# Performance work log

Measured on AMD Instinct MI355X. Metric: run time of the kernel, lower is better.

Reference implementation:

```python
import math
import jax, jax.numpy as jnp
import numpy as np

N_HEAD = 1
NORM_GROUPS = 32
EPS = 1e-5


def setup_inputs() -> dict:
    key = jax.random.key(0)
    ks = jax.random.split(key, 3)
    B, C, H, W, L = 4, 64, 16, 16, 16
    x = jax.random.normal(ks[0], (B, C, H, W, L), dtype=jnp.float32)
    gn_weight = jnp.ones((C,), dtype=jnp.float32)
    gn_bias = jnp.zeros((C,), dtype=jnp.float32)
    # 1x1x1 conv == per-voxel matmul; init like torch conv (kaiming-ish scale)
    qkv_weight = jax.random.normal(ks[1], (3 * C, C), dtype=jnp.float32) / math.sqrt(C)
    out_weight = jax.random.normal(ks[2], (C, C), dtype=jnp.float32) / math.sqrt(C)
    out_bias = jnp.zeros((C,), dtype=jnp.float32)
    return {"x": x, "gn_weight": gn_weight, "gn_bias": gn_bias,
            "qkv_weight": qkv_weight, "out_weight": out_weight, "out_bias": out_bias}


def _group_norm(x, w, b):
    B, C, H, W, L = x.shape
    g = NORM_GROUPS
    xg = x.reshape(B, g, C // g, H, W, L)
    mean = xg.mean(axis=(2, 3, 4, 5), keepdims=True)
    var = xg.var(axis=(2, 3, 4, 5), keepdims=True)
    xn = ((xg - mean) * jax.lax.rsqrt(var + EPS)).reshape(B, C, H, W, L)
    return xn * w[None, :, None, None, None] + b[None, :, None, None, None]


def reference(x, gn_weight, gn_bias, qkv_weight, out_weight, out_bias):
    B, C, H, W, L = x.shape
    n_head = N_HEAD
    head_dim = C // n_head
    N = H * W * L  # flattened voxel count

    norm = _group_norm(x, gn_weight, gn_bias)
    # 1x1x1 conv C -> 3C (no bias), then split heads
    qkv = jnp.einsum('bchwl,dc->bdhwl', norm, qkv_weight)
    qkv = qkv.reshape(B, n_head, 3 * head_dim, N)
    q, k, v = jnp.split(qkv, 3, axis=2)  # each [B, n_head, head_dim, N]

    # full N^2 attention; scale by sqrt(channel) as in the original (NOT head_dim)
    attn = jnp.einsum('bncq,bnck->bnqk', q, k) / math.sqrt(C)
    attn = jax.nn.softmax(attn, axis=-1)
    out = jnp.einsum('bnqk,bnck->bncq', attn, v).reshape(B, C, H, W, L)

    out = jnp.einsum('bchwl,dc->bdhwl', out, out_weight) + out_bias[None, :, None, None, None]
    return out + x
```

## Files before the change

### kernel.cpp

```cpp
#include <hip/hip_runtime.h>
#include <hip/hip_bf16.h>
#include <math.h>

#define BATCH 4
#define CH    64
#define NVOX  4096
#define NGRP  32
#define EPS   1e-5f

typedef float f32x4 __attribute__((ext_vector_type(4)));
typedef short s16x8 __attribute__((ext_vector_type(8)));

static __device__ inline unsigned short f2bf(float f) {
    union { __hip_bfloat16 h; unsigned short u; } cv;
    cv.h = __float2bfloat16(f);
    return cv.u;
}

__global__ __launch_bounds__(256) void k_gnstats(const float* __restrict__ x,
                                                 float* __restrict__ stats) {
    int bg = blockIdx.x;
    const float4* p4 = (const float4*)(x + (size_t)bg * (2 * NVOX));
    float s = 0.f, sq = 0.f;
    for (int i = threadIdx.x; i < (2 * NVOX) / 4; i += 256) {
        float4 v = p4[i];
        s  += v.x + v.y + v.z + v.w;
        sq += v.x * v.x + v.y * v.y + v.z * v.z + v.w * v.w;
    }
    for (int off = 32; off; off >>= 1) {
        s  += __shfl_down(s, off);
        sq += __shfl_down(sq, off);
    }
    __shared__ float ls[4], lq[4];
    int wid = threadIdx.x >> 6;
    if ((threadIdx.x & 63) == 0) { ls[wid] = s; lq[wid] = sq; }
    __syncthreads();
    if (threadIdx.x == 0) {
        s  = ls[0] + ls[1] + ls[2] + ls[3];
        sq = lq[0] + lq[1] + lq[2] + lq[3];
        float mean = s / (float)(2 * NVOX);
        float var  = sq / (float)(2 * NVOX) - mean * mean;
        stats[bg]       = mean;
        stats[128 + bg] = rsqrtf(var + EPS);
    }
}

__global__ __launch_bounds__(256) void k_qkv(const float* __restrict__ x,
                                             const float* __restrict__ stats,
                                             const float* __restrict__ gw,
                                             const float* __restrict__ gb,
                                             const float* __restrict__ W,
                                             unsigned short* __restrict__ Qb,
                                             unsigned short* __restrict__ Kb,
                                             unsigned short* __restrict__ Vb) {
    int b  = blockIdx.x >> 6;
    int n0 = (blockIdx.x & 63) * 64;
    int t  = threadIdx.x;
    __shared__ float nm[64][64];
    __shared__ alignas(16) unsigned short tb[64][72];

    for (int i = t; i < 64 * 16; i += 256) {
        int c = i >> 4;
        int n = (i & 15) * 4;
        float4 v = *(const float4*)&x[((size_t)(b * CH + c)) * NVOX + n0 + n];
        float mean = stats[b * NGRP + (c >> 1)];
        float rstd = stats[128 + b * NGRP + (c >> 1)];
        float sc = rstd * gw[c];
        float sh = gb[c] - mean * sc;
        nm[c][n + 0] = v.x * sc + sh;
        nm[c][n + 1] = v.y * sc + sh;
        nm[c][n + 2] = v.z * sc + sh;
        nm[c][n + 3] = v.w * sc + sh;
    }
    __syncthreads();

    int nl = t & 63;
    int dg = t >> 6;
    float r[64];
    #pragma unroll
    for (int c = 0; c < 64; ++c) r[c] = nm[c][nl];

    for (int j = 0; j < 16; ++j) {
        int d = dg * 16 + j;
        const float* w = &W[d * 64];
        float acc = 0.f;
        #pragma unroll
        for (int c = 0; c < 64; ++c) acc += w[c] * r[c];
        tb[nl][d] = f2bf(acc * 0.125f);
    }
    __syncthreads();
    {
        int n = t >> 2, d0 = (t & 3) * 16;
        s16x8 a0 = *(const s16x8*)&tb[n][d0];
        s16x8 a1 = *(const s16x8*)&tb[n][d0 + 8];
        size_t base = ((size_t)(b * NVOX + n0 + n)) * 64 + d0;
        *(s16x8*)&Qb[base]     = a0;
        *(s16x8*)&Qb[base + 8] = a1;
    }
    __syncthreads();

    for (int j = 0; j < 16; ++j) {
        int d = dg * 16 + j;
        const float* w = &W[(64 + d) * 64];
        float acc = 0.f;
        #pragma unroll
        for (int c = 0; c < 64; ++c) acc += w[c] * r[c];
        tb[nl][d] = f2bf(acc);
    }
    __syncthreads();
    {
        int n = t >> 2, d0 = (t & 3) * 16;
        s16x8 a0 = *(const s16x8*)&tb[n][d0];
        s16x8 a1 = *(const s16x8*)&tb[n][d0 + 8];
        size_t base = ((size_t)(b * NVOX + n0 + n)) * 64 + d0;
        *(s16x8*)&Kb[base]     = a0;
        *(s16x8*)&Kb[base + 8] = a1;
    }

    for (int j = 0; j < 16; ++j) {
        int d = dg * 16 + j;
        const float* w = &W[(128 + d) * 64];
        float acc = 0.f;
        #pragma unroll
        for (int c = 0; c < 64; ++c) acc += w[c] * r[c];
        Vb[((size_t)(b * 64 + d)) * NVOX + n0 + nl] = f2bf(acc);
    }
}

__global__ __launch_bounds__(256) void k_attn(const unsigned short* __restrict__ Qb,
                                              const unsigned short* __restrict__ Kb,
                                              const unsigned short* __restrict__ Vb,
                                              float* __restrict__ Obuf) {
    int b    = blockIdx.x >> 6;
    int q0   = (blockIdx.x & 63) * 64;
    int t    = threadIdx.x;
    int lane = t & 63;
    int w    = t >> 6;

    __shared__ alignas(16) unsigned short Ks[64][72];
    __shared__ alignas(16) unsigned short Vs[64][72];
    __shared__ alignas(16) unsigned short Ps[4][16][72];

    const unsigned short* Qp = Qb + (size_t)b * NVOX * 64;
    const unsigned short* Kp = Kb + (size_t)b * NVOX * 64;
    const unsigned short* Vp = Vb + (size_t)b * 64 * NVOX;

    int l15 = lane & 15;
    int g4  = lane >> 4;
    int csl = g4 * 8;
    int qrow = q0 + w * 16 + l15;
    s16x8 qf0 = *(const s16x8*)&Qp[(size_t)qrow * 64 + csl];
    s16x8 qf1 = *(const s16x8*)&Qp[(size_t)qrow * 64 + csl + 32];

    f32x4 acc_o[4] = {};
    float m_r[4], l_r[4];
    #pragma unroll
    for (int i = 0; i < 4; ++i) { m_r[i] = -1e30f; l_r[i] = 0.f; }

    int sr = t >> 2;
    int sc = (t & 3) * 16;

    s16x8 kr0, kr1, vr0, vr1;
    {
        const s16x8* pk = (const s16x8*)&Kp[(size_t)sr * 64 + sc];
        kr0 = pk[0]; kr1 = pk[1];
        const s16x8* pv = (const s16x8*)&Vp[(size_t)sr * NVOX + sc];
        vr0 = pv[0]; vr1 = pv[1];
    }

    for (int it = 0; it < NVOX / 64; ++it) {
        *(s16x8*)&Ks[sr][sc]     = kr0;
        *(s16x8*)&Ks[sr][sc + 8] = kr1;
        *(s16x8*)&Vs[sr][sc]     = vr0;
        *(s16x8*)&Vs[sr][sc + 8] = vr1;
        __syncthreads();

        if (it < NVOX / 64 - 1) {
            int k0n = (it + 1) * 64;
            const s16x8* pk = (const s16x8*)&Kp[((size_t)(k0n + sr)) * 64 + sc];
            kr0 = pk[0]; kr1 = pk[1];
            const s16x8* pv = (const s16x8*)&Vp[(size_t)sr * NVOX + k0n + sc];
            vr0 = pv[0]; vr1 = pv[1];
        }

        f32x4 sacc[4];
        #pragma unroll
        for (int kt = 0; kt < 4; ++kt) {
            s16x8 kf0 = *(const s16x8*)&Ks[kt * 16 + l15][csl];
            s16x8 kf1 = *(const s16x8*)&Ks[kt * 16 + l15][csl + 32];
            f32x4 z = {0.f, 0.f, 0.f, 0.f};
            sacc[kt] = __builtin_amdgcn_mfma_f32_16x16x32_bf16(qf0, kf0, z, 0, 0, 0);
            sacc[kt] = __builtin_amdgcn_mfma_f32_16x16x32_bf16(qf1, kf1, sacc[kt], 0, 0, 0);
        }

        float al[4];
        #pragma unroll
        for (int reg = 0; reg < 4; ++reg) {
            float rmax = fmaxf(fmaxf(sacc[0][reg], sacc[1][reg]),
                               fmaxf(sacc[2][reg], sacc[3][reg]));
            rmax = fmaxf(rmax, __shfl_xor(rmax, 1));
            rmax = fmaxf(rmax, __shfl_xor(rmax, 2));
            rmax = fmaxf(rmax, __shfl_xor(rmax, 4));
            rmax = fmaxf(rmax, __shfl_xor(rmax, 8));
            float mn = fmaxf(m_r[reg], rmax);
            al[reg] = __expf(m_r[reg] - mn);
            m_r[reg] = mn;
        }
        float p[4][4];
        #pragma unroll
        for (int kt = 0; kt < 4; ++kt)
            #pragma unroll
            for (int reg = 0; reg < 4; ++reg)
                p[kt][reg] = __expf(sacc[kt][reg] - m_r[reg]);
        #pragma unroll
        for (int reg = 0; reg < 4; ++reg) {
            float rs = p[0][reg] + p[1][reg] + p[2][reg] + p[3][reg];
            rs += __shfl_xor(rs, 1);
            rs += __shfl_xor(rs, 2);
            rs += __shfl_xor(rs, 4);
            rs += __shfl_xor(rs, 8);
            l_r[reg] = l_r[reg] * al[reg] + rs;
        }
        #pragma unroll
        for (int kt = 0; kt < 4; ++kt)
            #pragma unroll
            for (int reg = 0; reg < 4; ++reg)
                Ps[w][g4 * 4 + reg][kt * 16 + l15] = f2bf(p[kt][reg]);
        #pragma unroll
        for (int ct = 0; ct < 4; ++ct)
            #pragma unroll
            for (int reg = 0; reg < 4; ++reg)
                acc_o[ct][reg] *= al[reg];

        s16x8 pf0 = *(const s16x8*)&Ps[w][l15][csl];
        s16x8 pf1 = *(const s16x8*)&Ps[w][l15][csl + 32];
        #pragma unroll
        for (int ct = 0; ct < 4; ++ct) {
            s16x8 vf0 = *(const s16x8*)&Vs[ct * 16 + l15][csl];
            s16x8 vf1 = *(const s16x8*)&Vs[ct * 16 + l15][csl + 32];
            acc_o[ct] = __builtin_amdgcn_mfma_f32_16x16x32_bf16(pf0, vf0, acc_o[ct], 0, 0, 0);
            acc_o[ct] = __builtin_amdgcn_mfma_f32_16x16x32_bf16(pf1, vf1, acc_o[ct], 0, 0, 0);
        }
        __syncthreads();
    }

    float inv[4];
    #pragma unroll
    for (int reg = 0; reg < 4; ++reg) inv[reg] = 1.f / l_r[reg];
    #pragma unroll
    for (int ct = 0; ct < 4; ++ct)
        #pragma unroll
        for (int reg = 0; reg < 4; ++reg) {
            int q = q0 + w * 16 + g4 * 4 + reg;
            Obuf[((size_t)(b * NVOX + q)) * 64 + ct * 16 + l15] =
                acc_o[ct][reg] * inv[reg];
        }
}

__global__ __launch_bounds__(256) void k_outproj(const float* __restrict__ Obuf,
                                                 const float* __restrict__ Wout,
                                                 const float* __restrict__ obias,
                                                 const float* __restrict__ x,
                                                 float* __restrict__ out) {
    int b  = blockIdx.x >> 6;
    int n0 = (blockIdx.x & 63) * 64;
    int t  = threadIdx.x;
    __shared__ float os[64][65];
    for (int i = t; i < 64 * 16; i += 256) {
        int n  = i >> 4;
        int c4 = (i & 15) * 4;
        float4 v = *(const float4*)&Obuf[((size_t)(b * NVOX + n0 + n)) * 64 + c4];
        os[n][c4 + 0] = v.x; os[n][c4 + 1] = v.y;
        os[n][c4 + 2] = v.z; os[n][c4 + 3] = v.w;
    }
    __syncthreads();
    int nl = t & 63;
    int dg = t >> 6;
    float r[64];
    #pragma unroll
    for (int c = 0; c < 64; ++c) r[c] = os[nl][c];
    for (int j = 0; j < 16; ++j) {
        int d = dg * 16 + j;
        const float* wv = &Wout[d * 64];
        float acc = obias[d];
        #pragma unroll
        for (int c = 0; c < 64; ++c) acc += wv[c] * r[c];
        size_t idx = ((size_t)(b * CH + d)) * NVOX + n0 + nl;
        out[idx] = acc + x[idx];
    }
}

extern "C" void kernel_launch(void* const* d_in, const int* in_sizes, int n_in,
                              void* d_out, int out_size, void* d_ws, size_t ws_size,
                              hipStream_t stream) {
    const float* x     = (const float*)d_in[0];
    const float* gw    = (const float*)d_in[1];
    const float* gb    = (const float*)d_in[2];
    const float* Wqkv  = (const float*)d_in[3];
    const float* Wout  = (const float*)d_in[4];
    const float* obias = (const float*)d_in[5];
    float* out = (float*)d_out;

    float* ws    = (float*)d_ws;
    float* stats = ws;
    unsigned short* Qb = (unsigned short*)(ws + 256);
    unsigned short* Kb = Qb + (size_t)BATCH * NVOX * 64;
    unsigned short* Vb = Kb + (size_t)BATCH * NVOX * 64;
    float* Obuf = (float*)(Vb + (size_t)BATCH * NVOX * 64);

    k_gnstats<<<BATCH * NGRP, 256, 0, stream>>>(x, stats);
    k_qkv   <<<BATCH * 64,   256, 0, stream>>>(x, stats, gw, gb, Wqkv, Qb, Kb, Vb);
    k_attn  <<<BATCH * 64,   256, 0, stream>>>(Qb, Kb, Vb, Obuf);
    k_outproj<<<BATCH * 64,  256, 0, stream>>>(Obuf, Wout, obias, x, out);
}
```

Before: 196.2 us.

## Split attention KV range four ways and merge partials in output projection

Attention work is split across four KV chunks, so the grid grows from 256 to 1024 blocks and fills more of the GPU's compute units. Each block writes its unnormalized output plus running max and sum. The output-projection kernel then rescales and combines the four partials before the matmul. This adds workspace traffic for four fp32 partial outputs. The change also adds partial-unroll pragmas on the projection loops.

```diff
diff --git a/kernel.cpp b/kernel.cpp
--- a/kernel.cpp
+++ b/kernel.cpp
@@ -7,6 +7,8 @@
 #define NVOX  4096
 #define NGRP  32
 #define EPS   1e-5f
+#define SPLITS 4
+#define KVS   (NVOX / SPLITS)
 
 typedef float f32x4 __attribute__((ext_vector_type(4)));
 typedef short s16x8 __attribute__((ext_vector_type(8)));
@@ -80,6 +82,7 @@
     #pragma unroll
     for (int c = 0; c < 64; ++c) r[c] = nm[c][nl];
 
+    #pragma unroll 4
     for (int j = 0; j < 16; ++j) {
         int d = dg * 16 + j;
         const float* w = &W[d * 64];
@@ -99,6 +102,7 @@
     }
     __syncthreads();
 
+    #pragma unroll 4
     for (int j = 0; j < 16; ++j) {
         int d = dg * 16 + j;
         const float* w = &W[(64 + d) * 64];
@@ -117,6 +121,7 @@
         *(s16x8*)&Kb[base + 8] = a1;
     }
 
+    #pragma unroll 4
     for (int j = 0; j < 16; ++j) {
         int d = dg * 16 + j;
         const float* w = &W[(128 + d) * 64];
@@ -130,12 +135,17 @@
 __global__ __launch_bounds__(256) void k_attn(const unsigned short* __restrict__ Qb,
                                               const unsigned short* __restrict__ Kb,
                                               const unsigned short* __restrict__ Vb,
-                                              float* __restrict__ Obuf) {
-    int b    = blockIdx.x >> 6;
-    int q0   = (blockIdx.x & 63) * 64;
-    int t    = threadIdx.x;
-    int lane = t & 63;
-    int w    = t >> 6;
+                                              float* __restrict__ Opart,
+                                              float* __restrict__ Mpart,
+                                              float* __restrict__ Lpart) {
+    int split = blockIdx.x & 3;
+    int bq    = blockIdx.x >> 2;
+    int b     = bq >> 6;
+    int q0    = (bq & 63) * 64;
+    int t     = threadIdx.x;
+    int lane  = t & 63;
+    int w     = t >> 6;
+    const int kbase = split * KVS;
 
     __shared__ alignas(16) unsigned short Ks[64][72];
     __shared__ alignas(16) unsigned short Vs[64][72];
@@ -162,21 +172,21 @@
 
     s16x8 kr0, kr1, vr0, vr1;
     {
-        const s16x8* pk = (const s16x8*)&Kp[(size_t)sr * 64 + sc];
+        const s16x8* pk = (const s16x8*)&Kp[((size_t)(kbase + sr)) * 64 + sc];
         kr0 = pk[0]; kr1 = pk[1];
-        const s16x8* pv = (const s16x8*)&Vp[(size_t)sr * NVOX + sc];
+        const s16x8* pv = (const s16x8*)&Vp[(size_t)sr * NVOX + kbase + sc];
         vr0 = pv[0]; vr1 = pv[1];
     }
 
-    for (int it = 0; it < NVOX / 64; ++it) {
+    for (int it = 0; it < KVS / 64; ++it) {
         *(s16x8*)&Ks[sr][sc]     = kr0;
         *(s16x8*)&Ks[sr][sc + 8] = kr1;
         *(s16x8*)&Vs[sr][sc]     = vr0;
         *(s16x8*)&Vs[sr][sc + 8] = vr1;
         __syncthreads();
 
-        if (it < NVOX / 64 - 1) {
-            int k0n = (it + 1) * 64;
+        if (it < KVS / 64 - 1) {
+            int k0n = kbase + (it + 1) * 64;
             const s16x8* pk = (const s16x8*)&Kp[((size_t)(k0n + sr)) * 64 + sc];
             kr0 = pk[0]; kr1 = pk[1];
             const s16x8* pv = (const s16x8*)&Vp[(size_t)sr * NVOX + k0n + sc];
@@ -244,20 +254,27 @@
         __syncthreads();
     }
 
-    float inv[4];
-    #pragma unroll
-    for (int reg = 0; reg < 4; ++reg) inv[reg] = 1.f / l_r[reg];
     #pragma unroll
     for (int ct = 0; ct < 4; ++ct)
         #pragma unroll
         for (int reg = 0; reg < 4; ++reg) {
             int q = q0 + w * 16 + g4 * 4 + reg;
-            Obuf[((size_t)(b * NVOX + q)) * 64 + ct * 16 + l15] =
-                acc_o[ct][reg] * inv[reg];
-        }
-}
-
-__global__ __launch_bounds__(256) void k_outproj(const float* __restrict__ Obuf,
+            Opart[(((size_t)split * BATCH + b) * NVOX + q) * 64 + ct * 16 + l15] =
+                acc_o[ct][reg];
+        }
+    if (l15 == 0) {
+        #pragma unroll
+        for (int reg = 0; reg < 4; ++reg) {
+            int q = q0 + w * 16 + g4 * 4 + reg;
+            Mpart[((size_t)split * BATCH + b) * NVOX + q] = m_r[reg];
+            Lpart[((size_t)split * BATCH + b) * NVOX + q] = l_r[reg];
+        }
+    }
+}
+
+__global__ __launch_bounds__(256) void k_outproj(const float* __restrict__ Opart,
+                                                 const float* __restrict__ Mpart,
+                                                 const float* __restrict__ Lpart,
                                                  const float* __restrict__ Wout,
                                                  const float* __restrict__ obias,
                                                  const float* __restrict__ x,
@@ -266,19 +283,48 @@
     int n0 = (blockIdx.x & 63) * 64;
     int t  = threadIdx.x;
     __shared__ float os[64][65];
+    __shared__ float scs[64][4];
+
+    if (t < 64) {
+        size_t qg = (size_t)b * NVOX + n0 + t;
+        float m[SPLITS], l[SPLITS];
+        #pragma unroll
+        for (int s = 0; s < SPLITS; ++s) {
+            m[s] = Mpart[(size_t)s * BATCH * NVOX + qg];
+            l[s] = Lpart[(size_t)s * BATCH * NVOX + qg];
+        }
+        float mm = fmaxf(fmaxf(m[0], m[1]), fmaxf(m[2], m[3]));
+        float e[SPLITS], lsum = 0.f;
+        #pragma unroll
+        for (int s = 0; s < SPLITS; ++s) { e[s] = __expf(m[s] - mm); lsum += l[s] * e[s]; }
+        float inv = 1.f / lsum;
+        #pragma unroll
+        for (int s = 0; s < SPLITS; ++s) scs[t][s] = e[s] * inv;
+    }
+    __syncthreads();
+
     for (int i = t; i < 64 * 16; i += 256) {
         int n  = i >> 4;
         int c4 = (i & 15) * 4;
-        float4 v = *(const float4*)&Obuf[((size_t)(b * NVOX + n0 + n)) * 64 + c4];
-        os[n][c4 + 0] = v.x; os[n][c4 + 1] = v.y;
-        os[n][c4 + 2] = v.z; os[n][c4 + 3] = v.w;
-    }
-    __syncthreads();
+        size_t base = ((size_t)(b * NVOX + n0 + n)) * 64 + c4;
+        float4 a = {0.f, 0.f, 0.f, 0.f};
+        #pragma unroll
+        for (int s = 0; s < SPLITS; ++s) {
+            float4 v = *(const float4*)&Opart[(size_t)s * BATCH * NVOX * 64 + base];
+            float f = scs[n][s];
+            a.x += f * v.x; a.y += f * v.y; a.z += f * v.z; a.w += f * v.w;
+        }
+        os[n][c4 + 0] = a.x; os[n][c4 + 1] = a.y;
+        os[n][c4 + 2] = a.z; os[n][c4 + 3] = a.w;
+    }
+    __syncthreads();
+
     int nl = t & 63;
     int dg = t >> 6;
     float r[64];
     #pragma unroll
     for (int c = 0; c < 64; ++c) r[c] = os[nl][c];
+    #pragma unroll 4
     for (int j = 0; j < 16; ++j) {
         int d = dg * 16 + j;
         const float* wv = &Wout[d * 64];
@@ -306,10 +352,12 @@
     unsigned short* Qb = (unsigned short*)(ws + 256);
     unsigned short* Kb = Qb + (size_t)BATCH * NVOX * 64;
     unsigned short* Vb = Kb + (size_t)BATCH * NVOX * 64;
-    float* Obuf = (float*)(Vb + (size_t)BATCH * NVOX * 64);
-
-    k_gnstats<<<BATCH * NGRP, 256, 0, stream>>>(x, stats);
-    k_qkv   <<<BATCH * 64,   256, 0, stream>>>(x, stats, gw, gb, Wqkv, Qb, Kb, Vb);
-    k_attn  <<<BATCH * 64,   256, 0, stream>>>(Qb, Kb, Vb, Obuf);
-    k_outproj<<<BATCH * 64,  256, 0, stream>>>(Obuf, Wout, obias, x, out);
-}
+    float* Opart = (float*)(Vb + (size_t)BATCH * NVOX * 64);
+    float* Mpart = Opart + (size_t)SPLITS * BATCH * NVOX * 64;
+    float* Lpart = Mpart + (size_t)SPLITS * BATCH * NVOX;
+
+    k_gnstats<<<BATCH * NGRP,        256, 0, stream>>>(x, stats);
+    k_qkv   <<<BATCH * 64,           256, 0, stream>>>(x, stats, gw, gb, Wqkv, Qb, Kb, Vb);
+    k_attn  <<<BATCH * 64 * SPLITS,  256, 0, stream>>>(Qb, Kb, Vb, Opart, Mpart, Lpart);
+    k_outproj<<<BATCH * 64,          256, 0, stream>>>(Opart, Mpart, Lpart, Wout, obias, x, out);
+}
```

Result: faster. 190.7 us (-2.8%).

## Split KV across waves, fuse output projection into attention, read K/V directly

Applied to the files above, without the earlier changes.

The attention kernel now gives each block 16 queries, with the four waves each handling a quarter of the key range (split-K flash attention). K and V fragments are loaded straight from global memory, so the shared-memory staging and per-iteration barriers are gone. The partial results are then merged through shared memory with a log-sum-exp combine, and the output 1x1 projection, bias and residual are applied in the same kernel, which removes the Obuf round trip and one launch. The grid grows to 1024 blocks with an XCD-style block swizzle, and the QKV loops get partial unrolling. The risks are redundant global/L2 reads of K and V, since each block rereads the whole K/V of its batch, and extra per-block merge work.

```diff
diff --git a/kernel.cpp b/kernel.cpp
--- a/kernel.cpp
+++ b/kernel.cpp
@@ -80,6 +80,7 @@
     #pragma unroll
     for (int c = 0; c < 64; ++c) r[c] = nm[c][nl];
 
+    #pragma unroll 4
     for (int j = 0; j < 16; ++j) {
         int d = dg * 16 + j;
         const float* w = &W[d * 64];
@@ -99,6 +100,7 @@
     }
     __syncthreads();
 
+    #pragma unroll 4
     for (int j = 0; j < 16; ++j) {
         int d = dg * 16 + j;
         const float* w = &W[(64 + d) * 64];
@@ -117,6 +119,7 @@
         *(s16x8*)&Kb[base + 8] = a1;
     }
 
+    #pragma unroll 4
     for (int j = 0; j < 16; ++j) {
         int d = dg * 16 + j;
         const float* w = &W[(128 + d) * 64];
@@ -127,67 +130,52 @@
     }
 }
 
-__global__ __launch_bounds__(256) void k_attn(const unsigned short* __restrict__ Qb,
-                                              const unsigned short* __restrict__ Kb,
-                                              const unsigned short* __restrict__ Vb,
-                                              float* __restrict__ Obuf) {
-    int b    = blockIdx.x >> 6;
-    int q0   = (blockIdx.x & 63) * 64;
+__global__ __launch_bounds__(256) void k_attn_fused(const unsigned short* __restrict__ Qb,
+                                                    const unsigned short* __restrict__ Kb,
+                                                    const unsigned short* __restrict__ Vb,
+                                                    const float* __restrict__ Wout,
+                                                    const float* __restrict__ obias,
+                                                    const float* __restrict__ x,
+                                                    float* __restrict__ out) {
+    int bid = blockIdx.x;
+    int swz = (bid & 7) * 128 + (bid >> 3);
+    int b   = swz >> 8;
+    int q0  = (swz & 255) * 16;
+
     int t    = threadIdx.x;
     int lane = t & 63;
     int w    = t >> 6;
-
-    __shared__ alignas(16) unsigned short Ks[64][72];
-    __shared__ alignas(16) unsigned short Vs[64][72];
+    int l15  = lane & 15;
+    int g4   = lane >> 4;
+    int csl  = g4 * 8;
+
     __shared__ alignas(16) unsigned short Ps[4][16][72];
+    __shared__ float Part[4][16][68];
+    __shared__ float ml[4][2][16];
+    __shared__ float Os[16][68];
 
     const unsigned short* Qp = Qb + (size_t)b * NVOX * 64;
     const unsigned short* Kp = Kb + (size_t)b * NVOX * 64;
     const unsigned short* Vp = Vb + (size_t)b * 64 * NVOX;
 
-    int l15 = lane & 15;
-    int g4  = lane >> 4;
-    int csl = g4 * 8;
-    int qrow = q0 + w * 16 + l15;
-    s16x8 qf0 = *(const s16x8*)&Qp[(size_t)qrow * 64 + csl];
-    s16x8 qf1 = *(const s16x8*)&Qp[(size_t)qrow * 64 + csl + 32];
+    s16x8 qf0 = *(const s16x8*)&Qp[(size_t)(q0 + l15) * 64 + csl];
+    s16x8 qf1 = *(const s16x8*)&Qp[(size_t)(q0 + l15) * 64 + csl + 32];
 
     f32x4 acc_o[4] = {};
     float m_r[4], l_r[4];
     #pragma unroll
     for (int i = 0; i < 4; ++i) { m_r[i] = -1e30f; l_r[i] = 0.f; }
 
-    int sr = t >> 2;
-    int sc = (t & 3) * 16;
-
-    s16x8 kr0, kr1, vr0, vr1;
-    {
-        const s16x8* pk = (const s16x8*)&Kp[(size_t)sr * 64 + sc];
-        kr0 = pk[0]; kr1 = pk[1];
-        const s16x8* pv = (const s16x8*)&Vp[(size_t)sr * NVOX + sc];
-        vr0 = pv[0]; vr1 = pv[1];
-    }
-
-    for (int it = 0; it < NVOX / 64; ++it) {
-        *(s16x8*)&Ks[sr][sc]     = kr0;
-        *(s16x8*)&Ks[sr][sc + 8] = kr1;
-        *(s16x8*)&Vs[sr][sc]     = vr0;
-        *(s16x8*)&Vs[sr][sc + 8] = vr1;
-        __syncthreads();
-
-        if (it < NVOX / 64 - 1) {
-            int k0n = (it + 1) * 64;
-            const s16x8* pk = (const s16x8*)&Kp[((size_t)(k0n + sr)) * 64 + sc];
-            kr0 = pk[0]; kr1 = pk[1];
-            const s16x8* pv = (const s16x8*)&Vp[(size_t)sr * NVOX + k0n + sc];
-            vr0 = pv[0]; vr1 = pv[1];
-        }
+    const int kvbase = w * (NVOX / 4);
+
+    for (int it = 0; it < (NVOX / 4) / 64; ++it) {
+        int kv0 = kvbase + it * 64;
 
         f32x4 sacc[4];
         #pragma unroll
         for (int kt = 0; kt < 4; ++kt) {
-            s16x8 kf0 = *(const s16x8*)&Ks[kt * 16 + l15][csl];
-            s16x8 kf1 = *(const s16x8*)&Ks[kt * 16 + l15][csl + 32];
+            s16x8 kf0 = *(const s16x8*)&Kp[(size_t)(kv0 + kt * 16 + l15) * 64 + csl];
+            s16x8 kf1 = *(const s16x8*)&Kp[(size_t)(kv0 + kt * 16 + l15) * 64 + csl + 32];
             f32x4 z = {0.f, 0.f, 0.f, 0.f};
             sacc[kt] = __builtin_amdgcn_mfma_f32_16x16x32_bf16(qf0, kf0, z, 0, 0, 0);
             sacc[kt] = __builtin_amdgcn_mfma_f32_16x16x32_bf16(qf1, kf1, sacc[kt], 0, 0, 0);
@@ -236,57 +224,76 @@
         s16x8 pf1 = *(const s16x8*)&Ps[w][l15][csl + 32];
         #pragma unroll
         for (int ct = 0; ct < 4; ++ct) {
-            s16x8 vf0 = *(const s16x8*)&Vs[ct * 16 + l15][csl];
-            s16x8 vf1 = *(const s16x8*)&Vs[ct * 16 + l15][csl + 32];
+            s16x8 vf0 = *(const s16x8*)&Vp[(size_t)(ct * 16 + l15) * NVOX + kv0 + csl];
+            s16x8 vf1 = *(const s16x8*)&Vp[(size_t)(ct * 16 + l15) * NVOX + kv0 + csl + 32];
             acc_o[ct] = __builtin_amdgcn_mfma_f32_16x16x32_bf16(pf0, vf0, acc_o[ct], 0, 0, 0);
             acc_o[ct] = __builtin_amdgcn_mfma_f32_16x16x32_bf16(pf1, vf1, acc_o[ct], 0, 0, 0);
         }
-        __syncthreads();
-    }
-
-    float inv[4];
-    #pragma unroll
-    for (int reg = 0; reg < 4; ++reg) inv[reg] = 1.f / l_r[reg];
+    }
+
     #pragma unroll
     for (int ct = 0; ct < 4; ++ct)
         #pragma unroll
+        for (int reg = 0; reg < 4; ++reg)
+            Part[w][g4 * 4 + reg][ct * 16 + l15] = acc_o[ct][reg];
+    if (l15 == 0) {
+        #pragma unroll
         for (int reg = 0; reg < 4; ++reg) {
-            int q = q0 + w * 16 + g4 * 4 + reg;
-            Obuf[((size_t)(b * NVOX + q)) * 64 + ct * 16 + l15] =
-                acc_o[ct][reg] * inv[reg];
-        }
-}
-
-__global__ __launch_bounds__(256) void k_outproj(const float* __restrict__ Obuf,
-                                                 const float* __restrict__ Wout,
-                                                 const float* __restrict__ obias,
-                                                 const float* __restrict__ x,
-                                                 float* __restrict__ out) {
-    int b  = blockIdx.x >> 6;
-    int n0 = (blockIdx.x & 63) * 64;
-    int t  = threadIdx.x;
-    __shared__ float os[64][65];
-    for (int i = t; i < 64 * 16; i += 256) {
-        int n  = i >> 4;
-        int c4 = (i & 15) * 4;
-        float4 v = *(const float4*)&Obuf[((size_t)(b * NVOX + n0 + n)) * 64 + c4];
-        os[n][c4 + 0] = v.x; os[n][c4 + 1] = v.y;
-        os[n][c4 + 2] = v.z; os[n][c4 + 3] = v.w;
-    }
-    __syncthreads();
-    int nl = t & 63;
-    int dg = t >> 6;
-    float r[64];
-    #pragma unroll
-    for (int c = 0; c < 64; ++c) r[c] = os[nl][c];
-    for (int j = 0; j < 16; ++j) {
-        int d = dg * 16 + j;
-        const float* wv = &Wout[d * 64];
-        float acc = obias[d];
-        #pragma unroll
-        for (int c = 0; c < 64; ++c) acc += wv[c] * r[c];
-        size_t idx = ((size_t)(b * CH + d)) * NVOX + n0 + nl;
-        out[idx] = acc + x[idx];
+            ml[w][0][g4 * 4 + reg] = m_r[reg];
+            ml[w][1][g4 * 4 + reg] = l_r[reg];
+        }
+    }
+    __syncthreads();
+
+    {
+        int q  = t & 15;
+        int cg = t >> 4;
+        float m0 = ml[0][0][q], m1 = ml[1][0][q], m2 = ml[2][0][q], m3 = ml[3][0][q];
+        float mm = fmaxf(fmaxf(m0, m1), fmaxf(m2, m3));
+        float s0 = __expf(m0 - mm), s1 = __expf(m1 - mm);
+        float s2 = __expf(m2 - mm), s3 = __expf(m3 - mm);
+        float lsum = s0 * ml[0][1][q] + s1 * ml[1][1][q] +
+                     s2 * ml[2][1][q] + s3 * ml[3][1][q];
+        float inv = 1.f / lsum;
+        float4 o0 = *(const float4*)&Part[0][q][cg * 4];
+        float4 o1 = *(const float4*)&Part[1][q][cg * 4];
+        float4 o2 = *(const float4*)&Part[2][q][cg * 4];
+        float4 o3 = *(const float4*)&Part[3][q][cg * 4];
+        float4 o;
+        o.x = (s0 * o0.x + s1 * o1.x + s2 * o2.x + s3 * o3.x) * inv;
+        o.y = (s0 * o0.y + s1 * o1.y + s2 * o2.y + s3 * o3.y) * inv;
+        o.z = (s0 * o0.z + s1 * o1.z + s2 * o2.z + s3 * o3.z) * inv;
+        o.w = (s0 * o0.w + s1 * o1.w + s2 * o2.w + s3 * o3.w) * inv;
+        *(float4*)&Os[q][cg * 4] = o;
+    }
+    __syncthreads();
+
+    {
+        int q  = t & 15;
+        int dg = t >> 4;
+        int n  = q0 + q;
+        float a0 = obias[dg * 4 + 0], a1 = obias[dg * 4 + 1];
+        float a2 = obias[dg * 4 + 2], a3 = obias[dg * 4 + 3];
+        #pragma unroll
+        for (int c4 = 0; c4 < 16; ++c4) {
+            float4 ov = *(const float4*)&Os[q][c4 * 4];
+            float4 w0 = *(const float4*)&Wout[(size_t)(dg * 4 + 0) * 64 + c4 * 4];
+            float4 w1 = *(const float4*)&Wout[(size_t)(dg * 4 + 1) * 64 + c4 * 4];
+            float4 w2 = *(const float4*)&Wout[(size_t)(dg * 4 + 2) * 64 + c4 * 4];
+            float4 w3 = *(const float4*)&Wout[(size_t)(dg * 4 + 3) * 64 + c4 * 4];
+            a0 += w0.x * ov.x + w0.y * ov.y + w0.z * ov.z + w0.w * ov.w;
+            a1 += w1.x * ov.x + w1.y * ov.y + w1.z * ov.z + w1.w * ov.w;
+            a2 += w2.x * ov.x + w2.y * ov.y + w2.z * ov.z + w2.w * ov.w;
+            a3 += w3.x * ov.x + w3.y * ov.y + w3.z * ov.z + w3.w * ov.w;
+        }
+        size_t i0 = ((size_t)(b * CH + dg * 4 + 0)) * NVOX + n;
+        size_t i1 = ((size_t)(b * CH + dg * 4 + 1)) * NVOX + n;
+        size_t i2 = ((size_t)(b * CH + dg * 4 + 2)) * NVOX + n;
+        size_t i3 = ((size_t)(b * CH + dg * 4 + 3)) * NVOX + n;
+        out[i0] = a0 + x[i0];
+        out[i1] = a1 + x[i1];
+        out[i2] = a2 + x[i2];
+        out[i3] = a3 + x[i3];
     }
 }
 
@@ -306,10 +313,8 @@
     unsigned short* Qb = (unsigned short*)(ws + 256);
     unsigned short* Kb = Qb + (size_t)BATCH * NVOX * 64;
     unsigned short* Vb = Kb + (size_t)BATCH * NVOX * 64;
-    float* Obuf = (float*)(Vb + (size_t)BATCH * NVOX * 64);
-
-    k_gnstats<<<BATCH * NGRP, 256, 0, stream>>>(x, stats);
-    k_qkv   <<<BATCH * 64,   256, 0, stream>>>(x, stats, gw, gb, Wqkv, Qb, Kb, Vb);
-    k_attn  <<<BATCH * 64,   256, 0, stream>>>(Qb, Kb, Vb, Obuf);
-    k_outproj<<<BATCH * 64,  256, 0, stream>>>(Obuf, Wout, obias, x, out);
-}
+
+    k_gnstats   <<<BATCH * NGRP, 256, 0, stream>>>(x, stats);
+    k_qkv       <<<BATCH * 64,   256, 0, stream>>>(x, stats, gw, gb, Wqkv, Qb, Kb, Vb);
+    k_attn_fused<<<BATCH * 256,  256, 0, stream>>>(Qb, Kb, Vb, Wout, obias, x, out);
+}
```

After: 229.7 us. 17.1% more time.
